# Optimization experiments

Measured on AMD Instinct MI355X. Metric: run time of the kernel, lower is better.

## Reference

```python
import jax, jax.numpy as jnp
import numpy as np

# Faithful JAX port of MultiHeadSelfAttention.forward.
# Key observations about the torch code:
#  * einsum 'abcdef,ghdefi->abcdefi' with g=h=1 is a broadcast multiply:
#      U_hat_I[a,b,c,d,e,f,i] = U_hat[a,b,c,d,e,f] * W_affine[0,0,d,e,f,i]
#  * The per-i matmul loop builds A[...,e,e',i], but the follow-up einsum
#    'abcdeeg,abcdefg->abcdefg' only reads the DIAGONAL of A, i.e.
#      diag[...,e,i] = sum_f U_hat_I[...,e,f,i]^2 / sqrt(dim_capsules)
#    so we compute the diagonal directly (same math, no e x e intermediate).
#  * A_ = diag (broadcast over f) * W_t, then softmax over the f axis (dim=-2).

def setup_inputs() -> dict:
    key = jax.random.key(0)
    k1, k2, k3 = jax.random.split(key, 3)
    B, S1, S2, NC, DC, F, I = 32, 14, 14, 2, 16, 32, 8
    U_hat = jax.random.normal(k1, (B, S1, S2, NC, DC, F), dtype=jnp.float32)
    W_t = jax.random.normal(k2, (1, NC, DC, F, I), dtype=jnp.float32)
    W_affine = jax.random.normal(k3, (1, 1, NC, DC, F, I), dtype=jnp.float32)
    return {"U_hat": U_hat, "W_t": W_t, "W_affine": W_affine}


def reference(U_hat, W_t, W_affine):
    dim_capsules = U_hat.shape[4]
    d = jnp.sqrt(jnp.asarray(dim_capsules, dtype=U_hat.dtype))
    # (B,S1,S2,nc,dc,f,1) * (nc,dc,f,I) -> (B,S1,S2,nc,dc,f,I)
    U_hat_I = U_hat[..., None] * W_affine[0, 0]
    # diagonal of A_i = (X X^T)/sqrt(d): row-wise squared norm over f
    diag = jnp.sum(U_hat_I * U_hat_I, axis=-2) / d  # (B,S1,S2,nc,dc,I)
    # A_[a,b,c,d,e,f,i] = diag[a,b,c,d,e,i] * W_t[0,d,e,f,i]
    A_ = diag[..., None, :] * W_t[0]  # (B,S1,S2,nc,dc,f,I)
    C = jax.nn.softmax(A_, axis=-2)  # softmax over f (dim=-2)
    return (C, U_hat_I)
```

## Files before the change

kernel.cpp:

```cpp
#include <hip/hip_runtime.h>

#define N_ROWS      200704
#define ROW_ELEMS   256
#define C_ELEMS     51380224LL
#define BLOCKS      2048
#define WAVES_PER_BLOCK 4
#define TOTAL_WAVES (BLOCKS * WAVES_PER_BLOCK)

__global__ __launch_bounds__(256) void mhsa_softmax_kernel(
    const float* __restrict__ U_hat,
    const float* __restrict__ W_t,
    const float* __restrict__ W_affine,
    float* __restrict__ out)
{
    const int lane = threadIdx.x & 63;
    const int wid  = blockIdx.x * WAVES_PER_BLOCK + (threadIdx.x >> 6);
    const int q    = lane >> 2;
    const int de   = wid & 31;

    const float* wa = W_affine + de * ROW_ELEMS;
    const float* wt = W_t      + de * ROW_ELEMS;

    const int oA = 2 * lane;
    const int oB = 2 * lane + 128;

    const float2 wavA = *(const float2*)(wa + oA);
    const float2 wavB = *(const float2*)(wa + oB);
    const float2 wtvA = *(const float2*)(wt + oA);
    const float2 wtvB = *(const float2*)(wt + oB);

    float wtm0 = fmaxf(wtvA.x, wtvB.x);
    float wtm1 = fmaxf(wtvA.y, wtvB.y);
#pragma unroll
    for (int msk = 4; msk <= 32; msk <<= 1) {
        wtm0 = fmaxf(wtm0, __shfl_xor(wtm0, msk));
        wtm1 = fmaxf(wtm1, __shfl_xor(wtm1, msk));
    }

    int r = wid;
    float uA, uB;
    {
        const float* uh = U_hat + (long long)r * 32;
        uA = uh[q];
        uB = uh[q + 16];
    }

    while (r < N_ROWS) {
        const int rn = r + TOTAL_WAVES;
        const int rp = (rn < N_ROWS) ? rn : r;
        const float* uhn = U_hat + (long long)rp * 32;
        const float uAn = uhn[q];
        const float uBn = uhn[q + 16];

        float* outC = out + (long long)r * ROW_ELEMS;
        float* outU = out + C_ELEMS + (long long)r * ROW_ELEMS;

        float2 uhiA, uhiB;
        uhiA.x = uA * wavA.x;  uhiA.y = uA * wavA.y;
        uhiB.x = uB * wavB.x;  uhiB.y = uB * wavB.y;
        *(float2*)(outU + oA) = uhiA;
        *(float2*)(outU + oB) = uhiB;

        float p0 = fmaf(uhiA.x, uhiA.x, uhiB.x * uhiB.x);
        float p1 = fmaf(uhiA.y, uhiA.y, uhiB.y * uhiB.y);
#pragma unroll
        for (int msk = 4; msk <= 32; msk <<= 1) {
            p0 += __shfl_xor(p0, msk);
            p1 += __shfl_xor(p1, msk);
        }
        const float d0 = p0 * 0.25f;
        const float d1 = p1 * 0.25f;
        const float m0 = d0 * wtm0;
        const float m1 = d1 * wtm1;

        const float eAx = __expf(fmaf(d0, wtvA.x, -m0));
        const float eAy = __expf(fmaf(d1, wtvA.y, -m1));
        const float eBx = __expf(fmaf(d0, wtvB.x, -m0));
        const float eBy = __expf(fmaf(d1, wtvB.y, -m1));

        float s0 = eAx + eBx;
        float s1 = eAy + eBy;
#pragma unroll
        for (int msk = 4; msk <= 32; msk <<= 1) {
            s0 += __shfl_xor(s0, msk);
            s1 += __shfl_xor(s1, msk);
        }
        const float inv0 = __builtin_amdgcn_rcpf(s0);
        const float inv1 = __builtin_amdgcn_rcpf(s1);

        float2 cA, cB;
        cA.x = eAx * inv0;  cA.y = eAy * inv1;
        cB.x = eBx * inv0;  cB.y = eBy * inv1;
        *(float2*)(outC + oA) = cA;
        *(float2*)(outC + oB) = cB;

        uA = uAn;
        uB = uBn;
        r = rn;
    }
}

extern "C" void kernel_launch(void* const* d_in, const int* in_sizes, int n_in,
                              void* d_out, int out_size, void* d_ws, size_t ws_size,
                              hipStream_t stream) {
    const float* U_hat    = (const float*)d_in[0];
    const float* W_t      = (const float*)d_in[1];
    const float* W_affine = (const float*)d_in[2];
    float* out = (float*)d_out;

    mhsa_softmax_kernel<<<BLOCKS, 256, 0, stream>>>(U_hat, W_t, W_affine, out);
}
```

Measured before the change: 431.7 us.

## Give each wave a contiguous row range and stage weights in LDS

Each wave now handles a contiguous range of rows instead of a strided set, so its writes form long sequential streams. Because a wave now cycles through all 32 (nc,dc) weight slices, the kernel loads both weight tensors into shared memory once per block and precomputes per-column maxima of W_t there. The grid shrinks to 512 blocks, each using about 65 KB of LDS. This lowers occupancy and adds LDS reads on every row.

```diff
diff --git a/kernel.cpp b/kernel.cpp
--- a/kernel.cpp
+++ b/kernel.cpp
@@ -3,9 +3,10 @@
 #define N_ROWS      200704
 #define ROW_ELEMS   256
 #define C_ELEMS     51380224LL
-#define BLOCKS      2048
+#define BLOCKS      512
 #define WAVES_PER_BLOCK 4
 #define TOTAL_WAVES (BLOCKS * WAVES_PER_BLOCK)
+#define ROWS_PER_WAVE (N_ROWS / TOTAL_WAVES)
 
 __global__ __launch_bounds__(256) void mhsa_softmax_kernel(
     const float* __restrict__ U_hat,
@@ -13,31 +14,43 @@
     const float* __restrict__ W_affine,
     float* __restrict__ out)
 {
-    const int lane = threadIdx.x & 63;
-    const int wid  = blockIdx.x * WAVES_PER_BLOCK + (threadIdx.x >> 6);
+    __shared__ float lwa[32 * ROW_ELEMS];
+    __shared__ float lwt[32 * ROW_ELEMS];
+    __shared__ float lwm[32 * 8];
+
+    const int tid = threadIdx.x;
+
+    {
+        const float4* wa4 = (const float4*)W_affine;
+        const float4* wt4 = (const float4*)W_t;
+        float4* la4 = (float4*)lwa;
+        float4* lt4 = (float4*)lwt;
+#pragma unroll
+        for (int k = 0; k < 8; ++k) {
+            la4[tid + 256 * k] = wa4[tid + 256 * k];
+            lt4[tid + 256 * k] = wt4[tid + 256 * k];
+        }
+    }
+    __syncthreads();
+    {
+        const int de = tid >> 3, i = tid & 7;
+        float mx = lwt[de * 256 + i];
+        for (int f = 1; f < 32; ++f)
+            mx = fmaxf(mx, lwt[de * 256 + f * 8 + i]);
+        lwm[de * 8 + i] = mx;
+    }
+    __syncthreads();
+
+    const int lane = tid & 63;
+    const int wid  = blockIdx.x * WAVES_PER_BLOCK + (tid >> 6);
     const int q    = lane >> 2;
-    const int de   = wid & 31;
+    const int oA   = 2 * lane;
+    const int oB   = 2 * lane + 128;
+    const int i0   = 2 * (lane & 3);
 
-    const float* wa = W_affine + de * ROW_ELEMS;
-    const float* wt = W_t      + de * ROW_ELEMS;
+    int r = wid * ROWS_PER_WAVE;
+    const int rend = r + ROWS_PER_WAVE;
 
-    const int oA = 2 * lane;
-    const int oB = 2 * lane + 128;
-
-    const float2 wavA = *(const float2*)(wa + oA);
-    const float2 wavB = *(const float2*)(wa + oB);
-    const float2 wtvA = *(const float2*)(wt + oA);
-    const float2 wtvB = *(const float2*)(wt + oB);
-
-    float wtm0 = fmaxf(wtvA.x, wtvB.x);
-    float wtm1 = fmaxf(wtvA.y, wtvB.y);
-#pragma unroll
-    for (int msk = 4; msk <= 32; msk <<= 1) {
-        wtm0 = fmaxf(wtm0, __shfl_xor(wtm0, msk));
-        wtm1 = fmaxf(wtm1, __shfl_xor(wtm1, msk));
-    }
-
-    int r = wid;
     float uA, uB;
     {
         const float* uh = U_hat + (long long)r * 32;
@@ -45,12 +58,20 @@
         uB = uh[q + 16];
     }
 
-    while (r < N_ROWS) {
-        const int rn = r + TOTAL_WAVES;
-        const int rp = (rn < N_ROWS) ? rn : r;
+    for (; r < rend; ++r) {
+        const int rp = (r + 1 < rend) ? r + 1 : r;
         const float* uhn = U_hat + (long long)rp * 32;
         const float uAn = uhn[q];
         const float uBn = uhn[q + 16];
+
+        const int de = r & 31;
+        const float* wab = lwa + de * ROW_ELEMS;
+        const float* wtb = lwt + de * ROW_ELEMS;
+        const float2 wavA = *(const float2*)(wab + oA);
+        const float2 wavB = *(const float2*)(wab + oB);
+        const float2 wtvA = *(const float2*)(wtb + oA);
+        const float2 wtvB = *(const float2*)(wtb + oB);
+        const float2 wtm  = *(const float2*)(lwm + de * 8 + i0);
 
         float* outC = out + (long long)r * ROW_ELEMS;
         float* outU = out + C_ELEMS + (long long)r * ROW_ELEMS;
@@ -70,8 +91,8 @@
         }
         const float d0 = p0 * 0.25f;
         const float d1 = p1 * 0.25f;
-        const float m0 = d0 * wtm0;
-        const float m1 = d1 * wtm1;
+        const float m0 = d0 * wtm.x;
+        const float m1 = d1 * wtm.y;
 
         const float eAx = __expf(fmaf(d0, wtvA.x, -m0));
         const float eAy = __expf(fmaf(d1, wtvA.y, -m1));
@@ -96,7 +117,6 @@
 
         uA = uAn;
         uB = uBn;
-        r = rn;
     }
 }
 
```

New measurement: 468.9 us. 8.6% more time.
